# Kernel optimization log

Hardware: AMD Instinct MI355X
Metric: run time of the kernel (lower is better)

## Reference

```python
import jax, jax.numpy as jnp
import numpy as np

N, FEAT, K = 131072, 64, 2048  # points, features, clusters
DECAY = 0.99


def setup_inputs() -> dict:
    key = jax.random.key(0)
    k1, k2 = jax.random.split(key)
    x = jax.random.normal(k1, (N, FEAT), dtype=jnp.float32)
    centroids = jax.random.normal(k2, (K, FEAT), dtype=jnp.float32)
    return {"x": x, "centroids": centroids}


def reference(x, centroids):
    dists = (jnp.sum(x * x, axis=-1)[:, None]
             + jnp.sum(centroids * centroids, axis=-1)[None, :]
             - 2.0 * (x @ centroids.T))
    assignments = jnp.argmin(dists, axis=-1)  # [N] int

    # index_reduce 'mean' with include_self=False: scatter-mean of x into clusters;
    # clusters receiving no points keep their old centroid.
    k = centroids.shape[0]
    sums = jax.ops.segment_sum(x, assignments, num_segments=k)          # [K, FEAT]
    counts = jax.ops.segment_sum(jnp.ones((x.shape[0],), x.dtype),
                                 assignments, num_segments=k)           # [K]
    means = sums / jnp.maximum(counts, 1.0)[:, None]
    new_centroids = jnp.where(counts[:, None] > 0, means, centroids)

    # centroids.lerp_(new_centroids, 1 - decay)
    updated = DECAY * centroids + (1.0 - DECAY) * new_centroids
    return assignments, updated
```

## Files before the change

### kernel.cpp

```cpp
#include <hip/hip_runtime.h>
#include <math.h>

#define NPTS    131072
#define FEAT    64
#define KCLUS   2048
#define CHUNKC  256
#define NCHUNK  (KCLUS / CHUNKC)
#define PPW     32
#define WPB     4
#define PPB     (PPW * WPB)
#define CANDC   10

typedef __attribute__((ext_vector_type(8))) short frag_ab;
typedef __attribute__((ext_vector_type(4))) float frag_cd;

__device__ __forceinline__ short f2bf(float f) {
    unsigned u = __float_as_uint(f);
    u += 0x7FFFu + ((u >> 16) & 1u);
    return (short)(u >> 16);
}

__device__ __forceinline__ float exact_dist(const float* __restrict__ x,
                                            const float* __restrict__ c,
                                            float cnv, int p, int kk) {
    const float4* xr4 = (const float4*)&x[(size_t)p * FEAT];
    const float4* cr4 = (const float4*)&c[(size_t)kk * FEAT];
    float s = 0.f;
#pragma unroll
    for (int j = 0; j < 16; ++j) {
        float4 a4 = xr4[j], b4 = cr4[j];
        s = fmaf(a4.x, b4.x, s); s = fmaf(a4.y, b4.y, s);
        s = fmaf(a4.z, b4.z, s); s = fmaf(a4.w, b4.w, s);
    }
    return fmaf(-2.f, s, cnv);
}

__global__ void cprep_kernel(const float* __restrict__ c, float* __restrict__ cnorm,
                             short* __restrict__ cbs_t, float* __restrict__ cmax) {
    int k = blockIdx.x * blockDim.x + threadIdx.x;
    if (k >= KCLUS) return;
    const float4* row = (const float4*)&c[k * FEAT];
    float s = 0.f;
#pragma unroll
    for (int j = 0; j < 16; ++j) {
        float4 v = row[j];
        s = fmaf(v.x, v.x, s); s = fmaf(v.y, v.y, s);
        s = fmaf(v.z, v.z, s); s = fmaf(v.w, v.w, s);
        short4 b;
        b.x = f2bf(-2.f * v.x); b.y = f2bf(-2.f * v.y);
        b.z = f2bf(-2.f * v.z); b.w = f2bf(-2.f * v.w);
        *(short4*)&cbs_t[((size_t)(j >> 1) * KCLUS + k) * 8 + (j & 1) * 4] = b;
    }
    cnorm[k] = s;
    atomicMax((int*)cmax, __float_as_int(sqrtf(s)));
}

__device__ __forceinline__ void load_chunk(const short* __restrict__ cbs_t,
                                           const float* __restrict__ cnorm,
                                           int k0, int tid,
                                           frag_ab pre[8], float* cnpre) {
#pragma unroll
    for (int p8 = 0; p8 < 8; ++p8)
        pre[p8] = *(const frag_ab*)&cbs_t[((size_t)p8 * KCLUS + k0 + tid) * 8];
    *cnpre = cnorm[k0 + tid];
}

__global__ __launch_bounds__(256) void assign_kernel(
    const float* __restrict__ x, const float* __restrict__ c,
    const short* __restrict__ cbs_t, const float* __restrict__ cnorm,
    const float* __restrict__ cmaxp,
    float* __restrict__ out_assign, unsigned short* __restrict__ a16)
{
    __shared__ short csh[8 * CHUNKC * 8];
    __shared__ float cnsh[CHUNKC];

    const int tid = threadIdx.x, wv = tid >> 6, lane = tid & 63;
    const int col = lane & 15, q = lane >> 4;
    const int pt0 = blockIdx.x * PPB + wv * PPW;

    frag_ab A[2][2];
    float nrm[2];
#pragma unroll
    for (int rt = 0; rt < 2; ++rt) {
        float ps = 0.f;
#pragma unroll
        for (int kh = 0; kh < 2; ++kh) {
            const float4* xp = (const float4*)&x[(size_t)(pt0 + rt * 16 + col) * FEAT + kh * 32 + q * 8];
            float4 v0 = xp[0], v1 = xp[1];
            frag_ab a;
            a[0] = f2bf(v0.x); a[1] = f2bf(v0.y); a[2] = f2bf(v0.z); a[3] = f2bf(v0.w);
            a[4] = f2bf(v1.x); a[5] = f2bf(v1.y); a[6] = f2bf(v1.z); a[7] = f2bf(v1.w);
            A[rt][kh] = a;
            ps = fmaf(v0.x, v0.x, ps); ps = fmaf(v0.y, v0.y, ps);
            ps = fmaf(v0.z, v0.z, ps); ps = fmaf(v0.w, v0.w, ps);
            ps = fmaf(v1.x, v1.x, ps); ps = fmaf(v1.y, v1.y, ps);
            ps = fmaf(v1.z, v1.z, ps); ps = fmaf(v1.w, v1.w, ps);
        }
        ps += __shfl_xor(ps, 16);
        ps += __shfl_xor(ps, 32);
        nrm[rt] = sqrtf(ps);
    }

    float m[2][4];
#pragma unroll
    for (int rt = 0; rt < 2; ++rt)
#pragma unroll
        for (int r = 0; r < 4; ++r) m[rt][r] = INFINITY;

    frag_ab pre[8];
    float   cnpre;

    load_chunk(cbs_t, cnorm, 0, tid, pre, &cnpre);
    for (int c8 = 0; c8 < NCHUNK; ++c8) {
        __syncthreads();
#pragma unroll
        for (int p8 = 0; p8 < 8; ++p8)
            *(frag_ab*)&csh[(p8 * CHUNKC + tid) * 8] = pre[p8];
        cnsh[tid] = cnpre;
        __syncthreads();
        if (c8 < NCHUNK - 1)
            load_chunk(cbs_t, cnorm, (c8 + 1) * CHUNKC, tid, pre, &cnpre);

#pragma unroll 4
        for (int ct = 0; ct < CHUNKC / 16; ++ct) {
            const int lc = ct * 16 + col;
            frag_ab b0 = *(const frag_ab*)&csh[(q * CHUNKC + lc) * 8];
            frag_ab b1 = *(const frag_ab*)&csh[((4 + q) * CHUNKC + lc) * 8];
            const float cnv = cnsh[lc];
#pragma unroll
            for (int rt = 0; rt < 2; ++rt) {
                frag_cd acc = {cnv, cnv, cnv, cnv};
                acc = __builtin_amdgcn_mfma_f32_16x16x32_bf16(A[rt][0], b0, acc, 0, 0, 0);
                acc = __builtin_amdgcn_mfma_f32_16x16x32_bf16(A[rt][1], b1, acc, 0, 0, 0);
                m[rt][0] = fminf(m[rt][0], acc[0]);
                m[rt][1] = fminf(m[rt][1], acc[1]);
                m[rt][2] = fminf(m[rt][2], acc[2]);
                m[rt][3] = fminf(m[rt][3], acc[3]);
            }
        }
    }

    const float cmax = *cmaxp;
    float t[2][4];
#pragma unroll
    for (int rt = 0; rt < 2; ++rt)
#pragma unroll
        for (int r = 0; r < 4; ++r) {
            float mm = m[rt][r];
            mm = fminf(mm, __shfl_xor(mm, 1));
            mm = fminf(mm, __shfl_xor(mm, 2));
            mm = fminf(mm, __shfl_xor(mm, 4));
            mm = fminf(mm, __shfl_xor(mm, 8));
            float xnp = __shfl(nrm[rt], q * 4 + r);
            t[rt][r] = mm + 0.034f * xnp * cmax;
        }

    unsigned codes[CANDC];
    int ccnt = 0;

    load_chunk(cbs_t, cnorm, 0, tid, pre, &cnpre);
    for (int c8 = 0; c8 < NCHUNK; ++c8) {
        __syncthreads();
#pragma unroll
        for (int p8 = 0; p8 < 8; ++p8)
            *(frag_ab*)&csh[(p8 * CHUNKC + tid) * 8] = pre[p8];
        cnsh[tid] = cnpre;
        __syncthreads();
        if (c8 < NCHUNK - 1)
            load_chunk(cbs_t, cnorm, (c8 + 1) * CHUNKC, tid, pre, &cnpre);

        const int k0 = c8 * CHUNKC;
#pragma unroll 2
        for (int ct = 0; ct < CHUNKC / 16; ++ct) {
            const int lc = ct * 16 + col;
            frag_ab b0 = *(const frag_ab*)&csh[(q * CHUNKC + lc) * 8];
            frag_ab b1 = *(const frag_ab*)&csh[((4 + q) * CHUNKC + lc) * 8];
            const float cnv = cnsh[lc];
            const int kk = k0 + lc;
#pragma unroll
            for (int rt = 0; rt < 2; ++rt) {
                frag_cd acc = {cnv, cnv, cnv, cnv};
                acc = __builtin_amdgcn_mfma_f32_16x16x32_bf16(A[rt][0], b0, acc, 0, 0, 0);
                acc = __builtin_amdgcn_mfma_f32_16x16x32_bf16(A[rt][1], b1, acc, 0, 0, 0);
#pragma unroll
                for (int r = 0; r < 4; ++r) {
                    if (acc[r] <= t[rt][r]) {
                        unsigned code = ((unsigned)(rt * 16 + q * 4 + r) << 11) | (unsigned)kk;
#pragma unroll
                        for (int s = 0; s < CANDC; ++s)
                            if (s == ccnt) codes[s] = code;
                        ccnt++;
                    }
                }
            }
        }
    }

    const bool anyovf = __any(ccnt > CANDC);

    if (!anyovf) {
        float bestd[2][4];
        int   bestk[2][4];
#pragma unroll
        for (int rt = 0; rt < 2; ++rt)
#pragma unroll
            for (int r = 0; r < 4; ++r) { bestd[rt][r] = INFINITY; bestk[rt][r] = 0x7fffffff; }

        for (int i = 0; i < CANDC; ++i) {
            if (i < ccnt) {
                unsigned code = codes[i];
                int pl = (int)(code >> 11), kk = (int)(code & 2047u);
                float e = exact_dist(x, c, cnorm[kk], pt0 + pl, kk);
                int crt = pl >> 4, cr = pl & 3;
#pragma unroll
                for (int rt = 0; rt < 2; ++rt)
#pragma unroll
                    for (int r = 0; r < 4; ++r)
                        if (crt == rt && cr == r &&
                            (e < bestd[rt][r] || (e == bestd[rt][r] && kk < bestk[rt][r]))) {
                            bestd[rt][r] = e; bestk[rt][r] = kk;
                        }
            }
        }

#pragma unroll
        for (int rt = 0; rt < 2; ++rt) {
#pragma unroll
            for (int r = 0; r < 4; ++r) {
                float bd = bestd[rt][r]; int bk = bestk[rt][r];
#pragma unroll
                for (int mask = 1; mask <= 8; mask <<= 1) {
                    float od = __shfl_xor(bd, mask);
                    int   ok = __shfl_xor(bk, mask);
                    if (od < bd || (od == bd && ok < bk)) { bd = od; bk = ok; }
                }
                bestd[rt][r] = bd; bestk[rt][r] = bk;
            }
            if (col == 0) {
                float4 w = { (float)bestk[rt][0], (float)bestk[rt][1],
                             (float)bestk[rt][2], (float)bestk[rt][3] };
                *(float4*)&out_assign[pt0 + rt * 16 + q * 4] = w;
                ushort4 u = { (unsigned short)bestk[rt][0], (unsigned short)bestk[rt][1],
                              (unsigned short)bestk[rt][2], (unsigned short)bestk[rt][3] };
                *(ushort4*)&a16[pt0 + rt * 16 + q * 4] = u;
            }
        }
    } else {
        for (int pp = 0; pp < PPW; ++pp) {
            const int p = pt0 + pp;
            float bd = INFINITY; int bk = 0x7fffffff;
            for (int kk = lane; kk < KCLUS; kk += 64) {
                float e = exact_dist(x, c, cnorm[kk], p, kk);
                if (e < bd || (e == bd && kk < bk)) { bd = e; bk = kk; }
            }
#pragma unroll
            for (int mask = 1; mask <= 32; mask <<= 1) {
                float od = __shfl_xor(bd, mask);
                int   ok = __shfl_xor(bk, mask);
                if (od < bd || (od == bd && ok < bk)) { bd = od; bk = ok; }
            }
            if (lane == 0) {
                out_assign[p] = (float)bk;
                a16[p] = (unsigned short)bk;
            }
        }
    }
}

__global__ void scatter_kernel(const float* __restrict__ x,
                               const unsigned short* __restrict__ a16,
                               float* __restrict__ sums, int* __restrict__ counts) {
    __shared__ float wsum[4][8][64];
    __shared__ int   wcnt[4][8];

    const int tid = threadIdx.x, wv = tid >> 6, lane = tid & 63;
    const int c0 = blockIdx.x * 8;

    for (int idx = tid; idx < 4 * 8 * 64; idx += 256) ((float*)wsum)[idx] = 0.f;
    if (tid < 32) ((int*)wcnt)[tid] = 0;
    __syncthreads();

    const int base = blockIdx.y * 16384 + wv * 4096;
#pragma unroll 1
    for (int it = 0; it < 64; ++it) {
        const int pbase = base + it * 64;
        int a = (int)a16[pbase + lane];
        unsigned long long mask = __ballot(a >= c0 && a < c0 + 8);
        while (mask) {
            int j = __ffsll((long long)mask) - 1;
            mask &= mask - 1;
            int cl = __shfl(a, j) - c0;
            float xv = x[(size_t)(pbase + j) * FEAT + lane];
            wsum[wv][cl][lane] += xv;
            if (lane == 0) wcnt[wv][cl] += 1;
        }
    }
    __syncthreads();

    for (int idx = tid; idx < 512; idx += 256) {
        int cl = idx >> 6, ln = idx & 63;
        float s = wsum[0][cl][ln] + wsum[1][cl][ln] + wsum[2][cl][ln] + wsum[3][cl][ln];
        atomicAdd(&sums[(size_t)(c0 + cl) * FEAT + ln], s);
    }
    if (tid < 8) {
        int cc = wcnt[0][tid] + wcnt[1][tid] + wcnt[2][tid] + wcnt[3][tid];
        if (cc) atomicAdd(&counts[c0 + tid], cc);
    }
}

__global__ void update_kernel(const float* __restrict__ c,
                              const float* __restrict__ sums,
                              const int* __restrict__ counts,
                              float* __restrict__ out_upd) {
    int i = blockIdx.x * blockDim.x + threadIdx.x;
    if (i < KCLUS * FEAT) {
        int   k   = i >> 6;
        float cv  = c[i];
        int   cnt = counts[k];
        float nc  = (cnt > 0) ? (sums[i] / (float)cnt) : cv;
        out_upd[i] = 0.99f * cv + 0.01f * nc;
    }
}

extern "C" void kernel_launch(void* const* d_in, const int* in_sizes, int n_in,
                              void* d_out, int out_size, void* d_ws, size_t ws_size,
                              hipStream_t stream) {
    const float* x = (const float*)d_in[0];
    const float* c = (const float*)d_in[1];

    float* out        = (float*)d_out;
    float* out_assign = out;
    float* out_upd    = out + NPTS;

    char* ws = (char*)d_ws;
    constexpr size_t O_CNORM = 0;
    constexpr size_t O_CBS   = 8192;
    constexpr size_t O_ZERO  = 8192 + 262144;
    constexpr size_t O_CMAX  = O_ZERO;
    constexpr size_t O_SUMS  = O_ZERO + 64;
    constexpr size_t O_CNTS  = O_SUMS + 524288;
    constexpr size_t ZERO_LEN = 64 + 524288 + 8192;
    constexpr size_t O_A16   = O_ZERO + ZERO_LEN;

    float*    cnorm  = (float*)(ws + O_CNORM);
    short*    cbs_t  = (short*)(ws + O_CBS);
    float*    cmax   = (float*)(ws + O_CMAX);
    float*    sums   = (float*)(ws + O_SUMS);
    int*      counts = (int*)(ws + O_CNTS);
    unsigned short* a16 = (unsigned short*)(ws + O_A16);

    hipMemsetAsync(ws + O_ZERO, 0, ZERO_LEN, stream);

    cprep_kernel<<<KCLUS / 256, 256, 0, stream>>>(c, cnorm, cbs_t, cmax);
    assign_kernel<<<NPTS / PPB, 256, 0, stream>>>(x, c, cbs_t, cnorm, cmax,
                                                  out_assign, a16);
    scatter_kernel<<<dim3(KCLUS / 8, 8), 256, 0, stream>>>(x, a16, sums, counts);
    update_kernel<<<(KCLUS * FEAT) / 256, 256, 0, stream>>>(c, sums, counts, out_upd);
}
```

Measured before the change: 245.3 us.

## Double-buffer centroid chunks via direct global-to-LDS loads and double points per wave

After: 307.5 us. 1.25x slower.

```diff
diff --git a/kernel.cpp b/kernel.cpp
--- a/kernel.cpp
+++ b/kernel.cpp
@@ -6,10 +6,10 @@
 #define KCLUS   2048
 #define CHUNKC  256
 #define NCHUNK  (KCLUS / CHUNKC)
-#define PPW     32
+#define PPW     64
 #define WPB     4
 #define PPB     (PPW * WPB)
-#define CANDC   10
+#define CANDC   20
 
 typedef __attribute__((ext_vector_type(8))) short frag_ab;
 typedef __attribute__((ext_vector_type(4))) float frag_cd;
@@ -55,14 +55,18 @@
     atomicMax((int*)cmax, __float_as_int(sqrtf(s)));
 }
 
-__device__ __forceinline__ void load_chunk(const short* __restrict__ cbs_t,
-                                           const float* __restrict__ cnorm,
-                                           int k0, int tid,
-                                           frag_ab pre[8], float* cnpre) {
-#pragma unroll
-    for (int p8 = 0; p8 < 8; ++p8)
-        pre[p8] = *(const frag_ab*)&cbs_t[((size_t)p8 * KCLUS + k0 + tid) * 8];
-    *cnpre = cnorm[k0 + tid];
+__device__ __forceinline__ void stage_chunk(const short* __restrict__ cbs_t,
+                                            short* dst, int k0, int wv, int lane) {
+#pragma unroll
+    for (int j = 0; j < 8; ++j) {
+        const int e = (wv * 8 + j) * 64 + lane;
+        const int p = e >> 8, cc = e & 255;
+        const short* g = &cbs_t[((size_t)p * KCLUS + k0 + cc) * 8];
+        short* l = &dst[(size_t)e * 8];
+        __builtin_amdgcn_global_load_lds(
+            (const __attribute__((address_space(1))) unsigned int*)g,
+            (__attribute__((address_space(3))) unsigned int*)l, 16, 0, 0);
+    }
 }
 
 __global__ __launch_bounds__(256) void assign_kernel(
@@ -71,17 +75,18 @@
     const float* __restrict__ cmaxp,
     float* __restrict__ out_assign, unsigned short* __restrict__ a16)
 {
-    __shared__ short csh[8 * CHUNKC * 8];
-    __shared__ float cnsh[CHUNKC];
+    __shared__ short csh[2][8 * CHUNKC * 8];
 
     const int tid = threadIdx.x, wv = tid >> 6, lane = tid & 63;
     const int col = lane & 15, q = lane >> 4;
     const int pt0 = blockIdx.x * PPB + wv * PPW;
 
-    frag_ab A[2][2];
-    float nrm[2];
-#pragma unroll
-    for (int rt = 0; rt < 2; ++rt) {
+    stage_chunk(cbs_t, &csh[0][0], 0, wv, lane);
+
+    frag_ab A[4][2];
+    float nrm[4];
+#pragma unroll
+    for (int rt = 0; rt < 4; ++rt) {
         float ps = 0.f;
 #pragma unroll
         for (int kh = 0; kh < 2; ++kh) {
@@ -101,34 +106,27 @@
         nrm[rt] = sqrtf(ps);
     }
 
-    float m[2][4];
-#pragma unroll
-    for (int rt = 0; rt < 2; ++rt)
+    float m[4][4];
+#pragma unroll
+    for (int rt = 0; rt < 4; ++rt)
 #pragma unroll
         for (int r = 0; r < 4; ++r) m[rt][r] = INFINITY;
 
-    frag_ab pre[8];
-    float   cnpre;
-
-    load_chunk(cbs_t, cnorm, 0, tid, pre, &cnpre);
+    __syncthreads();
+
     for (int c8 = 0; c8 < NCHUNK; ++c8) {
-        __syncthreads();
-#pragma unroll
-        for (int p8 = 0; p8 < 8; ++p8)
-            *(frag_ab*)&csh[(p8 * CHUNKC + tid) * 8] = pre[p8];
-        cnsh[tid] = cnpre;
-        __syncthreads();
-        if (c8 < NCHUNK - 1)
-            load_chunk(cbs_t, cnorm, (c8 + 1) * CHUNKC, tid, pre, &cnpre);
-
-#pragma unroll 4
+        const int cur = c8 & 1;
+        stage_chunk(cbs_t, &csh[cur ^ 1][0], ((c8 + 1) & 7) * CHUNKC, wv, lane);
+        const short* cbuf = &csh[cur][0];
+        const int k0 = c8 * CHUNKC;
+#pragma unroll 2
         for (int ct = 0; ct < CHUNKC / 16; ++ct) {
             const int lc = ct * 16 + col;
-            frag_ab b0 = *(const frag_ab*)&csh[(q * CHUNKC + lc) * 8];
-            frag_ab b1 = *(const frag_ab*)&csh[((4 + q) * CHUNKC + lc) * 8];
-            const float cnv = cnsh[lc];
-#pragma unroll
-            for (int rt = 0; rt < 2; ++rt) {
+            frag_ab b0 = *(const frag_ab*)&cbuf[(q * CHUNKC + lc) * 8];
+            frag_ab b1 = *(const frag_ab*)&cbuf[((4 + q) * CHUNKC + lc) * 8];
+            const float cnv = cnorm[k0 + lc];
+#pragma unroll
+            for (int rt = 0; rt < 4; ++rt) {
                 frag_cd acc = {cnv, cnv, cnv, cnv};
                 acc = __builtin_amdgcn_mfma_f32_16x16x32_bf16(A[rt][0], b0, acc, 0, 0, 0);
                 acc = __builtin_amdgcn_mfma_f32_16x16x32_bf16(A[rt][1], b1, acc, 0, 0, 0);
@@ -138,12 +136,13 @@
                 m[rt][3] = fminf(m[rt][3], acc[3]);
             }
         }
+        __syncthreads();
     }
 
     const float cmax = *cmaxp;
-    float t[2][4];
-#pragma unroll
-    for (int rt = 0; rt < 2; ++rt)
+    float t[4][4];
+#pragma unroll
+    for (int rt = 0; rt < 4; ++rt)
 #pragma unroll
         for (int r = 0; r < 4; ++r) {
             float mm = m[rt][r];
@@ -158,27 +157,20 @@
     unsigned codes[CANDC];
     int ccnt = 0;
 
-    load_chunk(cbs_t, cnorm, 0, tid, pre, &cnpre);
     for (int c8 = 0; c8 < NCHUNK; ++c8) {
-        __syncthreads();
-#pragma unroll
-        for (int p8 = 0; p8 < 8; ++p8)
-            *(frag_ab*)&csh[(p8 * CHUNKC + tid) * 8] = pre[p8];
-        cnsh[tid] = cnpre;
-        __syncthreads();
-        if (c8 < NCHUNK - 1)
-            load_chunk(cbs_t, cnorm, (c8 + 1) * CHUNKC, tid, pre, &cnpre);
-
+        const int cur = c8 & 1;
+        stage_chunk(cbs_t, &csh[cur ^ 1][0], ((c8 + 1) & 7) * CHUNKC, wv, lane);
+        const short* cbuf = &csh[cur][0];
         const int k0 = c8 * CHUNKC;
 #pragma unroll 2
         for (int ct = 0; ct < CHUNKC / 16; ++ct) {
             const int lc = ct * 16 + col;
-            frag_ab b0 = *(const frag_ab*)&csh[(q * CHUNKC + lc) * 8];
-            frag_ab b1 = *(const frag_ab*)&csh[((4 + q) * CHUNKC + lc) * 8];
-            const float cnv = cnsh[lc];
+            frag_ab b0 = *(const frag_ab*)&cbuf[(q * CHUNKC + lc) * 8];
+            frag_ab b1 = *(const frag_ab*)&cbuf[((4 + q) * CHUNKC + lc) * 8];
+            const float cnv = cnorm[k0 + lc];
             const int kk = k0 + lc;
 #pragma unroll
-            for (int rt = 0; rt < 2; ++rt) {
+            for (int rt = 0; rt < 4; ++rt) {
                 frag_cd acc = {cnv, cnv, cnv, cnv};
                 acc = __builtin_amdgcn_mfma_f32_16x16x32_bf16(A[rt][0], b0, acc, 0, 0, 0);
                 acc = __builtin_amdgcn_mfma_f32_16x16x32_bf16(A[rt][1], b1, acc, 0, 0, 0);
@@ -194,15 +186,16 @@
                 }
             }
         }
+        __syncthreads();
     }
 
     const bool anyovf = __any(ccnt > CANDC);
 
     if (!anyovf) {
-        float bestd[2][4];
-        int   bestk[2][4];
-#pragma unroll
-        for (int rt = 0; rt < 2; ++rt)
+        float bestd[4][4];
+        int   bestk[4][4];
+#pragma unroll
+        for (int rt = 0; rt < 4; ++rt)
 #pragma unroll
             for (int r = 0; r < 4; ++r) { bestd[rt][r] = INFINITY; bestk[rt][r] = 0x7fffffff; }
 
@@ -213,7 +206,7 @@
                 float e = exact_dist(x, c, cnorm[kk], pt0 + pl, kk);
                 int crt = pl >> 4, cr = pl & 3;
 #pragma unroll
-                for (int rt = 0; rt < 2; ++rt)
+                for (int rt = 0; rt < 4; ++rt)
 #pragma unroll
                     for (int r = 0; r < 4; ++r)
                         if (crt == rt && cr == r &&
@@ -224,7 +217,7 @@
         }
 
 #pragma unroll
-        for (int rt = 0; rt < 2; ++rt) {
+        for (int rt = 0; rt < 4; ++rt) {
 #pragma unroll
             for (int r = 0; r < 4; ++r) {
                 float bd = bestd[rt][r]; int bk = bestk[rt][r];
```

## Split first-pass min search across wave pairs with 64-row tiles per wave

Applied to the files above, without the earlier changes.

Result: slower. 326.9 us (+33.3%).

```diff
diff --git a/kernel.cpp b/kernel.cpp
--- a/kernel.cpp
+++ b/kernel.cpp
@@ -76,21 +76,23 @@
 
     const int tid = threadIdx.x, wv = tid >> 6, lane = tid & 63;
     const int col = lane & 15, q = lane >> 4;
-    const int pt0 = blockIdx.x * PPB + wv * PPW;
-
-    frag_ab A[2][2];
-    float nrm[2];
-#pragma unroll
-    for (int rt = 0; rt < 2; ++rt) {
+    const int pt0  = blockIdx.x * PPB + wv * PPW;
+    const int pt0p = blockIdx.x * PPB + (wv >> 1) * 64;
+    const int h = wv & 1;
+
+    frag_ab A4[4][2];
+    float nrm4[4];
+#pragma unroll
+    for (int rt = 0; rt < 4; ++rt) {
         float ps = 0.f;
 #pragma unroll
         for (int kh = 0; kh < 2; ++kh) {
-            const float4* xp = (const float4*)&x[(size_t)(pt0 + rt * 16 + col) * FEAT + kh * 32 + q * 8];
+            const float4* xp = (const float4*)&x[(size_t)(pt0p + rt * 16 + col) * FEAT + kh * 32 + q * 8];
             float4 v0 = xp[0], v1 = xp[1];
             frag_ab a;
             a[0] = f2bf(v0.x); a[1] = f2bf(v0.y); a[2] = f2bf(v0.z); a[3] = f2bf(v0.w);
             a[4] = f2bf(v1.x); a[5] = f2bf(v1.y); a[6] = f2bf(v1.z); a[7] = f2bf(v1.w);
-            A[rt][kh] = a;
+            A4[rt][kh] = a;
             ps = fmaf(v0.x, v0.x, ps); ps = fmaf(v0.y, v0.y, ps);
             ps = fmaf(v0.z, v0.z, ps); ps = fmaf(v0.w, v0.w, ps);
             ps = fmaf(v1.x, v1.x, ps); ps = fmaf(v1.y, v1.y, ps);
@@ -98,14 +100,14 @@
         }
         ps += __shfl_xor(ps, 16);
         ps += __shfl_xor(ps, 32);
-        nrm[rt] = sqrtf(ps);
-    }
-
-    float m[2][4];
-#pragma unroll
-    for (int rt = 0; rt < 2; ++rt)
-#pragma unroll
-        for (int r = 0; r < 4; ++r) m[rt][r] = INFINITY;
+        nrm4[rt] = sqrtf(ps);
+    }
+
+    float m4[4][4];
+#pragma unroll
+    for (int rt = 0; rt < 4; ++rt)
+#pragma unroll
+        for (int r = 0; r < 4; ++r) m4[rt][r] = INFINITY;
 
     frag_ab pre[8];
     float   cnpre;
@@ -122,38 +124,63 @@
             load_chunk(cbs_t, cnorm, (c8 + 1) * CHUNKC, tid, pre, &cnpre);
 
 #pragma unroll 4
-        for (int ct = 0; ct < CHUNKC / 16; ++ct) {
-            const int lc = ct * 16 + col;
+        for (int ct = 0; ct < CHUNKC / 32; ++ct) {
+            const int lc = h * 128 + ct * 16 + col;
             frag_ab b0 = *(const frag_ab*)&csh[(q * CHUNKC + lc) * 8];
             frag_ab b1 = *(const frag_ab*)&csh[((4 + q) * CHUNKC + lc) * 8];
             const float cnv = cnsh[lc];
 #pragma unroll
-            for (int rt = 0; rt < 2; ++rt) {
+            for (int rt = 0; rt < 4; ++rt) {
                 frag_cd acc = {cnv, cnv, cnv, cnv};
-                acc = __builtin_amdgcn_mfma_f32_16x16x32_bf16(A[rt][0], b0, acc, 0, 0, 0);
-                acc = __builtin_amdgcn_mfma_f32_16x16x32_bf16(A[rt][1], b1, acc, 0, 0, 0);
-                m[rt][0] = fminf(m[rt][0], acc[0]);
-                m[rt][1] = fminf(m[rt][1], acc[1]);
-                m[rt][2] = fminf(m[rt][2], acc[2]);
-                m[rt][3] = fminf(m[rt][3], acc[3]);
-            }
+                acc = __builtin_amdgcn_mfma_f32_16x16x32_bf16(A4[rt][0], b0, acc, 0, 0, 0);
+                acc = __builtin_amdgcn_mfma_f32_16x16x32_bf16(A4[rt][1], b1, acc, 0, 0, 0);
+                m4[rt][0] = fminf(m4[rt][0], acc[0]);
+                m4[rt][1] = fminf(m4[rt][1], acc[1]);
+                m4[rt][2] = fminf(m4[rt][2], acc[2]);
+                m4[rt][3] = fminf(m4[rt][3], acc[3]);
+            }
+        }
+    }
+
+    __syncthreads();
+    {
+        float* mx = (float*)csh;
+#pragma unroll
+        for (int rt = 0; rt < 4; ++rt) {
+            float4 v = { m4[rt][0], m4[rt][1], m4[rt][2], m4[rt][3] };
+            *(float4*)&mx[tid * 16 + rt * 4] = v;
+        }
+    }
+    __syncthreads();
+    {
+        const float* mx = (const float*)csh;
+        const int ptid = tid ^ 64;
+#pragma unroll
+        for (int rt = 0; rt < 4; ++rt) {
+            float4 v = *(const float4*)&mx[ptid * 16 + rt * 4];
+            m4[rt][0] = fminf(m4[rt][0], v.x);
+            m4[rt][1] = fminf(m4[rt][1], v.y);
+            m4[rt][2] = fminf(m4[rt][2], v.z);
+            m4[rt][3] = fminf(m4[rt][3], v.w);
         }
     }
 
     const float cmax = *cmaxp;
     float t[2][4];
 #pragma unroll
-    for (int rt = 0; rt < 2; ++rt)
+    for (int rt = 0; rt < 2; ++rt) {
+        const int art = h * 2 + rt;
 #pragma unroll
         for (int r = 0; r < 4; ++r) {
-            float mm = m[rt][r];
+            float mm = m4[art][r];
             mm = fminf(mm, __shfl_xor(mm, 1));
             mm = fminf(mm, __shfl_xor(mm, 2));
             mm = fminf(mm, __shfl_xor(mm, 4));
             mm = fminf(mm, __shfl_xor(mm, 8));
-            float xnp = __shfl(nrm[rt], q * 4 + r);
+            float xnp = __shfl(nrm4[art], q * 4 + r);
             t[rt][r] = mm + 0.034f * xnp * cmax;
         }
+    }
 
     unsigned codes[CANDC];
     int ccnt = 0;
@@ -180,8 +207,8 @@
 #pragma unroll
             for (int rt = 0; rt < 2; ++rt) {
                 frag_cd acc = {cnv, cnv, cnv, cnv};
-                acc = __builtin_amdgcn_mfma_f32_16x16x32_bf16(A[rt][0], b0, acc, 0, 0, 0);
-                acc = __builtin_amdgcn_mfma_f32_16x16x32_bf16(A[rt][1], b1, acc, 0, 0, 0);
+                acc = __builtin_amdgcn_mfma_f32_16x16x32_bf16(A4[h * 2 + rt][0], b0, acc, 0, 0, 0);
+                acc = __builtin_amdgcn_mfma_f32_16x16x32_bf16(A4[h * 2 + rt][1], b1, acc, 0, 0, 0);
 #pragma unroll
                 for (int r = 0; r < 4; ++r) {
                     if (acc[r] <= t[rt][r]) {
```

## Fuse two-pass min/candidate scan into single pass with running threshold

Applied to the files above, without the earlier changes.

Measured after the change: 367.6 us. +49.9%, slower.

```diff
diff --git a/kernel.cpp b/kernel.cpp
--- a/kernel.cpp
+++ b/kernel.cpp
@@ -9,7 +9,7 @@
 #define PPW     32
 #define WPB     4
 #define PPB     (PPW * WPB)
-#define CANDC   10
+#define CANDC   20
 
 typedef __attribute__((ext_vector_type(8))) short frag_ab;
 typedef __attribute__((ext_vector_type(4))) float frag_cd;
@@ -101,73 +101,80 @@
         nrm[rt] = sqrtf(ps);
     }
 
-    float m[2][4];
+    const float cmax = *cmaxp;
+    float marg[2][4];
 #pragma unroll
     for (int rt = 0; rt < 2; ++rt)
 #pragma unroll
+        for (int r = 0; r < 4; ++r)
+            marg[rt][r] = 0.034f * __shfl(nrm[rt], q * 4 + r) * cmax;
+
+    float m[2][4], t[2][4];
+#pragma unroll
+    for (int rt = 0; rt < 2; ++rt)
+#pragma unroll
         for (int r = 0; r < 4; ++r) m[rt][r] = INFINITY;
+
+#define REFRESH_T()                                                    \
+    do {                                                               \
+        _Pragma("unroll")                                              \
+        for (int rt = 0; rt < 2; ++rt) {                               \
+            _Pragma("unroll")                                          \
+            for (int r = 0; r < 4; ++r) {                              \
+                float mm = m[rt][r];                                   \
+                mm = fminf(mm, __shfl_xor(mm, 1));                     \
+                mm = fminf(mm, __shfl_xor(mm, 2));                     \
+                mm = fminf(mm, __shfl_xor(mm, 4));                     \
+                mm = fminf(mm, __shfl_xor(mm, 8));                     \
+                t[rt][r] = mm + marg[rt][r];                           \
+            }                                                          \
+        }                                                              \
+    } while (0)
 
     frag_ab pre[8];
     float   cnpre;
 
-    load_chunk(cbs_t, cnorm, 0, tid, pre, &cnpre);
-    for (int c8 = 0; c8 < NCHUNK; ++c8) {
-        __syncthreads();
-#pragma unroll
-        for (int p8 = 0; p8 < 8; ++p8)
-            *(frag_ab*)&csh[(p8 * CHUNKC + tid) * 8] = pre[p8];
-        cnsh[tid] = cnpre;
-        __syncthreads();
-        if (c8 < NCHUNK - 1)
-            load_chunk(cbs_t, cnorm, (c8 + 1) * CHUNKC, tid, pre, &cnpre);
-
-#pragma unroll 4
-        for (int ct = 0; ct < CHUNKC / 16; ++ct) {
-            const int lc = ct * 16 + col;
-            frag_ab b0 = *(const frag_ab*)&csh[(q * CHUNKC + lc) * 8];
-            frag_ab b1 = *(const frag_ab*)&csh[((4 + q) * CHUNKC + lc) * 8];
-            const float cnv = cnsh[lc];
-#pragma unroll
-            for (int rt = 0; rt < 2; ++rt) {
-                frag_cd acc = {cnv, cnv, cnv, cnv};
-                acc = __builtin_amdgcn_mfma_f32_16x16x32_bf16(A[rt][0], b0, acc, 0, 0, 0);
-                acc = __builtin_amdgcn_mfma_f32_16x16x32_bf16(A[rt][1], b1, acc, 0, 0, 0);
-                m[rt][0] = fminf(m[rt][0], acc[0]);
-                m[rt][1] = fminf(m[rt][1], acc[1]);
-                m[rt][2] = fminf(m[rt][2], acc[2]);
-                m[rt][3] = fminf(m[rt][3], acc[3]);
-            }
-        }
-    }
-
-    const float cmax = *cmaxp;
-    float t[2][4];
-#pragma unroll
-    for (int rt = 0; rt < 2; ++rt)
-#pragma unroll
-        for (int r = 0; r < 4; ++r) {
-            float mm = m[rt][r];
-            mm = fminf(mm, __shfl_xor(mm, 1));
-            mm = fminf(mm, __shfl_xor(mm, 2));
-            mm = fminf(mm, __shfl_xor(mm, 4));
-            mm = fminf(mm, __shfl_xor(mm, 8));
-            float xnp = __shfl(nrm[rt], q * 4 + r);
-            t[rt][r] = mm + 0.034f * xnp * cmax;
-        }
-
     unsigned codes[CANDC];
     int ccnt = 0;
 
     load_chunk(cbs_t, cnorm, 0, tid, pre, &cnpre);
+#pragma unroll
+    for (int p8 = 0; p8 < 8; ++p8)
+        *(frag_ab*)&csh[(p8 * CHUNKC + tid) * 8] = pre[p8];
+    cnsh[tid] = cnpre;
+    __syncthreads();
+    load_chunk(cbs_t, cnorm, CHUNKC, tid, pre, &cnpre);
+
+#pragma unroll 4
+    for (int ct = 0; ct < CHUNKC / 16; ++ct) {
+        const int lc = ct * 16 + col;
+        frag_ab b0 = *(const frag_ab*)&csh[(q * CHUNKC + lc) * 8];
+        frag_ab b1 = *(const frag_ab*)&csh[((4 + q) * CHUNKC + lc) * 8];
+        const float cnv = cnsh[lc];
+#pragma unroll
+        for (int rt = 0; rt < 2; ++rt) {
+            frag_cd acc = {cnv, cnv, cnv, cnv};
+            acc = __builtin_amdgcn_mfma_f32_16x16x32_bf16(A[rt][0], b0, acc, 0, 0, 0);
+            acc = __builtin_amdgcn_mfma_f32_16x16x32_bf16(A[rt][1], b1, acc, 0, 0, 0);
+            m[rt][0] = fminf(m[rt][0], acc[0]);
+            m[rt][1] = fminf(m[rt][1], acc[1]);
+            m[rt][2] = fminf(m[rt][2], acc[2]);
+            m[rt][3] = fminf(m[rt][3], acc[3]);
+        }
+    }
+    REFRESH_T();
+
     for (int c8 = 0; c8 < NCHUNK; ++c8) {
-        __syncthreads();
-#pragma unroll
-        for (int p8 = 0; p8 < 8; ++p8)
-            *(frag_ab*)&csh[(p8 * CHUNKC + tid) * 8] = pre[p8];
-        cnsh[tid] = cnpre;
-        __syncthreads();
-        if (c8 < NCHUNK - 1)
-            load_chunk(cbs_t, cnorm, (c8 + 1) * CHUNKC, tid, pre, &cnpre);
+        if (c8 > 0) {
+            __syncthreads();
+#pragma unroll
+            for (int p8 = 0; p8 < 8; ++p8)
+                *(frag_ab*)&csh[(p8 * CHUNKC + tid) * 8] = pre[p8];
+            cnsh[tid] = cnpre;
+            __syncthreads();
+            if (c8 < NCHUNK - 1)
+                load_chunk(cbs_t, cnorm, (c8 + 1) * CHUNKC, tid, pre, &cnpre);
+        }
 
         const int k0 = c8 * CHUNKC;
 #pragma unroll 2
@@ -184,6 +191,7 @@
                 acc = __builtin_amdgcn_mfma_f32_16x16x32_bf16(A[rt][1], b1, acc, 0, 0, 0);
 #pragma unroll
                 for (int r = 0; r < 4; ++r) {
+                    m[rt][r] = fminf(m[rt][r], acc[r]);
                     if (acc[r] <= t[rt][r]) {
                         unsigned code = ((unsigned)(rt * 16 + q * 4 + r) << 11) | (unsigned)kk;
 #pragma unroll
@@ -194,6 +202,7 @@
                 }
             }
         }
+        if (c8 < NCHUNK - 1) REFRESH_T();
     }
 
     const bool anyovf = __any(ccnt > CANDC);
```
